# Kernel tuning notes

Measured on AMD Instinct MI355X. Metric: run time of the kernel, lower is better.

The kernel has to match this reference:

```python
import jax, jax.numpy as jnp
import numpy as np

# Action space: 3 discrete action types, 8 options each (MultiDiscrete nvec)
ACTION_NUMS = np.array([8, 8, 8])
A_TOTAL = int(ACTION_NUMS.sum())          # 24
START_IDX = np.cumsum([0, *ACTION_NUMS[:-1]])  # [0, 8, 16]
F, N, D = 4096, 64, 256                   # frames, agents(actions per frame), feat_size
HID = 140                                 # fixed in ForwardNet


def setup_inputs() -> dict:
    key = jax.random.key(0)
    ks = jax.random.split(key, 8)
    s = lambda fan_in: 1.0 / np.sqrt(fan_in)
    return {
        "current_feature": jax.random.normal(ks[0], (F, N, D), jnp.float32),
        "next_feature": jax.random.normal(ks[1], (F, N, D), jnp.float32),
        "actions": jax.random.randint(ks[2], (F, 3, N), 0, 8, dtype=jnp.int32),
        "W1": jax.random.normal(ks[3], (D + A_TOTAL, HID), jnp.float32) * s(D + A_TOTAL),
        "b1": jnp.zeros((HID,), jnp.float32),
        "W2": jax.random.normal(ks[4], (HID, D), jnp.float32) * s(HID),
        "b2": jnp.zeros((D,), jnp.float32),
        "Wi": jax.random.normal(ks[5], (2 * D, A_TOTAL), jnp.float32) * s(2 * D),
        "bi": jnp.zeros((A_TOTAL,), jnp.float32),
    }


def actions2onehot(actions):
    # actions: [F, T, N] int. Vectorized replacement for the triple Python loop:
    # each (frame, agent) row gets a 1 at START_IDX[type] + action, per type.
    start = jnp.asarray(START_IDX, actions.dtype)          # [T]
    idx = actions + start[None, :, None]                    # [F, T, N]
    oh = jax.nn.one_hot(idx, A_TOTAL, dtype=jnp.float32)    # [F, T, N, A]
    return oh.sum(axis=1)                                   # [F, N, A] (column ranges disjoint)


def reference(current_feature, next_feature, actions, W1, b1, W2, b2, Wi, bi):
    action_one_hot = actions2onehot(actions)                       # [F, N, 24]
    # Forward dynamics (attn_target != ICM branch)
    fwd_in = jnp.concatenate([current_feature, action_one_hot], axis=2)  # [F, N, 280]
    h = jax.nn.leaky_relu(fwd_in @ W1 + b1, negative_slope=0.1)
    next_feature_pred = h @ W2 + b2                                # [F, N, 256]
    # Inverse dynamics
    inv_in = jnp.concatenate([current_feature, next_feature], axis=2)   # [F, N, 512]
    action_pred = inv_in @ Wi + bi                                 # [F, N, 24] per-type logits concatenated
    return next_feature_pred, action_pred
```

## Files before the change

kernel.cpp:

```cpp
#include <hip/hip_runtime.h>
#include <hip/hip_bf16.h>
#include <stdint.h>


typedef __attribute__((ext_vector_type(8))) short short8;
typedef __attribute__((ext_vector_type(4))) float float4v;

#define MFMA16 __builtin_amdgcn_mfma_f32_16x16x32_bf16

__device__ __align__(16) uint16_t g_wpack[98816];

__device__ __forceinline__ uint16_t f2bf(float f) {
    __hip_bfloat16 h = __float2bfloat16(f);
    return *reinterpret_cast<uint16_t*>(&h);
}

__device__ __forceinline__ short8 cvt8(float4v x0, float4v x1) {
    union { __hip_bfloat162 b2[4]; short8 s; } u;
    u.b2[0] = __float22bfloat162_rn(make_float2(x0[0], x0[1]));
    u.b2[1] = __float22bfloat162_rn(make_float2(x0[2], x0[3]));
    u.b2[2] = __float22bfloat162_rn(make_float2(x1[0], x1[1]));
    u.b2[3] = __float22bfloat162_rn(make_float2(x1[2], x1[3]));
    return u.s;
}

__global__ __launch_bounds__(256) void pack_weights(
    const float* __restrict__ W1, const float* __restrict__ W2,
    const float* __restrict__ Wi)
{
    int e = blockIdx.x * 256 + threadIdx.x;
    const float* W; int NT, Kr, Nr, ld, le, base;
    if (e < 41472)      { W = W1; NT = 9;  Kr = 280; Nr = 140; ld = 140; le = e;         base = 0; }
    else if (e < 82432) { W = W2; NT = 16; Kr = 140; Nr = 256; ld = 256; le = e - 41472; base = 41472; }
    else if (e < 98816) { W = Wi; NT = 2;  Kr = 512; Nr = 24;  ld = 24;  le = e - 82432; base = 82432; }
    else return;
    int i = le & 7, lane = (le >> 3) & 63, frag = le >> 9;
    int kt = frag / NT, nt = frag - kt * NT;
    int k = kt * 32 + ((lane >> 4) << 3) + i;
    int n = nt * 16 + (lane & 15);
    float v = (k < Kr && n < Nr) ? W[k * ld + n] : 0.0f;
    g_wpack[base + le] = f2bf(v);
}

__global__ __launch_bounds__(256, 2) void icm_main(
    const float* __restrict__ cf, const float* __restrict__ nf,
    const int* __restrict__ act,
    const float* __restrict__ b1, const float* __restrict__ b2,
    const float* __restrict__ bi,
    float* __restrict__ out)
{
    __shared__ char smem[73728];

    const int tid  = threadIdx.x;
    const int wave = tid >> 6;
    const int lane = tid & 63;
    const int lhi  = lane >> 4;
    const int llo  = lane & 15;
    char* hA   = smem + wave * 8192;
    char* hB   = smem + 32768 + wave * 2048;
    char* wstA = smem + 40960;
    char* wstB = smem + 57344;

    const long rowbase = (long)blockIdx.x * 128 + wave * 32;

    short8 wreg[4];

    auto ld_stage1 = [&](int kt) {
        const char* w1b = (const char*)(g_wpack + kt * 9 * 512);
        const char* wib = (const char*)(g_wpack + 82432 + kt * 2 * 512);
        const int nb = (kt == 8) ? 9216 : 11264;
        #pragma unroll
        for (int k = 0; k < 3; ++k) {
            int b = k * 4096 + tid * 16;
            if (b < nb)
                wreg[k] = (b < 9216) ? *(const short8*)(w1b + b)
                                     : *(const short8*)(wib + (b - 9216));
        }
    };
    auto st_stage1 = [&](char* dst, int kt) {
        const int nb = (kt == 8) ? 9216 : 11264;
        #pragma unroll
        for (int k = 0; k < 3; ++k) {
            int b = k * 4096 + tid * 16;
            if (b < nb) *(short8*)(dst + b) = wreg[k];
        }
    };
    auto ld_stage_c = [&](const uint16_t* src) {
        #pragma unroll
        for (int k = 0; k < 4; ++k)
            wreg[k] = *(const short8*)((const char*)src + k * 4096 + tid * 16);
    };
    auto st_stage_c = [&](char* dst) {
        #pragma unroll
        for (int k = 0; k < 4; ++k)
            *(short8*)(dst + k * 4096 + tid * 16) = wreg[k];
    };

    int i0[2], i1[2], i2[2];
    #pragma unroll
    for (int m = 0; m < 2; ++m) {
        long r = rowbase + m * 16 + llo;
        long f = r >> 6; int n = (int)(r & 63);
        i0[m] = act[(f * 3 + 0) * 64 + n];
        i1[m] = act[(f * 3 + 1) * 64 + n] + 8;
        i2[m] = act[(f * 3 + 2) * 64 + n] + 16;
    }

    const float4v fz = {0.f, 0.f, 0.f, 0.f};
    float4v acc1[2][9];
    float4v acc3[2][2];
    #pragma unroll
    for (int m = 0; m < 2; ++m) {
        #pragma unroll
        for (int n = 0; n < 9; ++n) acc1[m][n] = fz;
        acc3[m][0] = fz; acc3[m][1] = fz;
    }

    const float* cfb[2];
    #pragma unroll
    for (int m = 0; m < 2; ++m)
        cfb[m] = cf + (rowbase + m * 16 + llo) * 256 + lhi * 8;

    float4v pa0[2], pa1[2];
    ld_stage1(0);
    #pragma unroll
    for (int m = 0; m < 2; ++m) {
        pa0[m] = *(const float4v*)(cfb[m]);
        pa1[m] = *(const float4v*)(cfb[m] + 4);
    }
    st_stage1(wstA, 0);
    __syncthreads();

    #pragma unroll 1
    for (int kt = 0; kt < 9; ++kt) {
        if (kt < 8) ld_stage1(kt + 1);
        const char* wb = (kt & 1) ? wstB : wstA;

        short8 a[2];
        if (kt < 8) {
            a[0] = cvt8(pa0[0], pa1[0]);
            a[1] = cvt8(pa0[1], pa1[1]);
            if (kt < 7) {
                #pragma unroll
                for (int m = 0; m < 2; ++m) {
                    pa0[m] = *(const float4v*)(cfb[m] + (kt + 1) * 32);
                    pa1[m] = *(const float4v*)(cfb[m] + (kt + 1) * 32 + 4);
                }
            }
        } else {
            #pragma unroll
            for (int m = 0; m < 2; ++m) {
                #pragma unroll
                for (int i = 0; i < 8; ++i) {
                    int kk = lhi * 8 + i;
                    a[m][i] = (kk == i0[m] || kk == i1[m] || kk == i2[m])
                                  ? (short)0x3F80 : (short)0;
                }
            }
        }

        #pragma unroll
        for (int nt = 0; nt < 9; ++nt) {
            short8 bf = *(const short8*)(wb + (nt << 10) + (lane << 4));
            acc1[0][nt] = MFMA16(a[0], bf, acc1[0][nt], 0, 0, 0);
            acc1[1][nt] = MFMA16(a[1], bf, acc1[1][nt], 0, 0, 0);
        }
        if (kt < 8) {
            #pragma unroll
            for (int nt = 0; nt < 2; ++nt) {
                short8 bf = *(const short8*)(wb + ((9 + nt) << 10) + (lane << 4));
                acc3[0][nt] = MFMA16(a[0], bf, acc3[0][nt], 0, 0, 0);
                acc3[1][nt] = MFMA16(a[1], bf, acc3[1][nt], 0, 0, 0);
            }
            st_stage1(((kt + 1) & 1) ? wstB : wstA, kt + 1);
        }
        __syncthreads();
    }

    ld_stage_c(g_wpack + 82432 + (16 << 9));

    #pragma unroll
    for (int m = 0; m < 2; ++m) {
        #pragma unroll
        for (int nt = 0; nt < 9; ++nt) {
            int col = nt * 16 + llo;
            float bb = b1[col < 140 ? col : 139];
            #pragma unroll
            for (int r = 0; r < 4; ++r) {
                float v = acc1[m][nt][r] + bb;
                v = v > 0.f ? v : 0.1f * v;
                int row = m * 16 + lhi * 4 + r;
                if (nt < 8) {
                    int off = row * 256 + ((col * 2) ^ ((row & 7) << 4));
                    *(uint16_t*)(hA + off) = f2bf(v);
                } else {
                    int off = row * 64 + (((col - 128) * 2) ^ ((row & 3) << 4));
                    *(uint16_t*)(hB + off) = f2bf(v);
                }
            }
        }
    }
    #pragma unroll
    for (int z = 0; z < 4; ++z) {
        int zz  = lane * 4 + z;
        int row = zz >> 3, d = zz & 7;
        int off = row * 64 + ((32 + d * 4) ^ ((row & 3) << 4));
        *(int*)(hB + off) = 0;
    }

    st_stage_c(wstB);

    const float* nfb[2];
    #pragma unroll
    for (int m = 0; m < 2; ++m)
        nfb[m] = nf + (rowbase + m * 16 + llo) * 256 + lhi * 8;
    #pragma unroll
    for (int m = 0; m < 2; ++m) {
        pa0[m] = *(const float4v*)(nfb[m]);
        pa1[m] = *(const float4v*)(nfb[m] + 4);
    }
    __syncthreads();

    ld_stage_c(g_wpack + 41472);
    #pragma unroll 1
    for (int kt = 0; kt < 8; ++kt) {
        short8 a[2];
        a[0] = cvt8(pa0[0], pa1[0]);
        a[1] = cvt8(pa0[1], pa1[1]);
        if (kt < 7) {
            #pragma unroll
            for (int m = 0; m < 2; ++m) {
                pa0[m] = *(const float4v*)(nfb[m] + (kt + 1) * 32);
                pa1[m] = *(const float4v*)(nfb[m] + (kt + 1) * 32 + 4);
            }
        }
        #pragma unroll
        for (int nt = 0; nt < 2; ++nt) {
            short8 bf = *(const short8*)(wstB + (((kt << 1) + nt) << 10) + (lane << 4));
            acc3[0][nt] = MFMA16(a[0], bf, acc3[0][nt], 0, 0, 0);
            acc3[1][nt] = MFMA16(a[1], bf, acc3[1][nt], 0, 0, 0);
        }
    }
    float* out2 = out + 67108864L;
    #pragma unroll
    for (int m = 0; m < 2; ++m) {
        #pragma unroll
        for (int nt = 0; nt < 2; ++nt) {
            int col = nt * 16 + llo;
            if (col < 24) {
                float bb = bi[col];
                #pragma unroll
                for (int r = 0; r < 4; ++r) {
                    long row = rowbase + m * 16 + lhi * 4 + r;
                    out2[row * 24 + col] = acc3[m][nt][r] + bb;
                }
            }
        }
    }
    st_stage_c(wstA);
    __syncthreads();

    float4v acc2[2][16];
    #pragma unroll
    for (int m = 0; m < 2; ++m)
        #pragma unroll
        for (int n = 0; n < 16; ++n) acc2[m][n] = fz;

    #pragma unroll 1
    for (int kt = 0; kt < 5; ++kt) {
        if (kt < 4) ld_stage_c(g_wpack + 41472 + ((kt + 1) << 13));
        const char* wb = (kt & 1) ? wstB : wstA;

        short8 a[2];
        #pragma unroll
        for (int m = 0; m < 2; ++m) {
            int row = m * 16 + llo;
            if (kt < 4) {
                int off = row * 256 + ((kt * 64 + lhi * 16) ^ ((row & 7) << 4));
                a[m] = *(const short8*)(hA + off);
            } else {
                int off = row * 64 + ((lhi * 16) ^ ((row & 3) << 4));
                a[m] = *(const short8*)(hB + off);
            }
        }
        #pragma unroll
        for (int nt = 0; nt < 16; ++nt) {
            short8 bf = *(const short8*)(wb + (nt << 10) + (lane << 4));
            acc2[0][nt] = MFMA16(a[0], bf, acc2[0][nt], 0, 0, 0);
            acc2[1][nt] = MFMA16(a[1], bf, acc2[1][nt], 0, 0, 0);
        }
        if (kt < 4) st_stage_c(((kt + 1) & 1) ? wstB : wstA);
        __syncthreads();
    }

    #pragma unroll
    for (int m = 0; m < 2; ++m) {
        #pragma unroll
        for (int n = 0; n < 16; ++n) {
            int col = n * 16 + llo;
            float bb = b2[col];
            #pragma unroll
            for (int r = 0; r < 4; ++r) {
                long row = rowbase + m * 16 + lhi * 4 + r;
                out[row * 256 + col] = acc2[m][n][r] + bb;
            }
        }
    }
}

extern "C" void kernel_launch(void* const* d_in, const int* in_sizes, int n_in,
                              void* d_out, int out_size, void* d_ws, size_t ws_size,
                              hipStream_t stream) {
    const float *cf = nullptr, *nf = nullptr, *W1 = nullptr, *b1 = nullptr;
    const float *W2 = nullptr, *b2 = nullptr, *Wi = nullptr, *bi = nullptr;
    const int *ac = nullptr;
    for (int i = 0; i < n_in; ++i) {
        int s = in_sizes[i];
        const void* p = d_in[i];
        switch (s) {
            case 67108864: if (!cf) cf = (const float*)p; else nf = (const float*)p; break;
            case 786432:   ac = (const int*)p;   break;
            case 39200:    W1 = (const float*)p; break;
            case 140:      b1 = (const float*)p; break;
            case 35840:    W2 = (const float*)p; break;
            case 256:      b2 = (const float*)p; break;
            case 12288:    Wi = (const float*)p; break;
            case 24:       bi = (const float*)p; break;
            default: break;
        }
    }
    float* ob = (float*)d_out;

    pack_weights<<<386, 256, 0, stream>>>(W1, W2, Wi);
    icm_main<<<2048, 256, 0, stream>>>(cf, nf, ac, b1, b2, bi, ob);
}
```

Measured before the change: 205.2 us.

## Stage weights via direct global-to-LDS loads and double-buffer activation prefetch

Replaces the register round-trip for weight staging (global load into VGPRs, then LDS store) with global_load_lds async copies issued per wave. Activation loads now use two alternating register sets, so rows are prefetched two k-steps ahead, and bias values are hoisted into registers. The one-hot k-step is peeled out of the main loop. This aims to free registers and hide global latency better. The risk is ordering and visibility of the LDS copies, which rely on the existing barriers to be complete.

```diff
diff --git a/kernel.cpp b/kernel.cpp
--- a/kernel.cpp
+++ b/kernel.cpp
@@ -9,6 +9,12 @@
 #define MFMA16 __builtin_amdgcn_mfma_f32_16x16x32_bf16
 
 __device__ __align__(16) uint16_t g_wpack[98816];
+
+__device__ __forceinline__ void gl_lds16(const void* g, void* l) {
+    __builtin_amdgcn_global_load_lds(
+        (const __attribute__((address_space(1))) unsigned int*)g,
+        (__attribute__((address_space(3))) unsigned int*)l, 16, 0, 0);
+}
 
 __device__ __forceinline__ uint16_t f2bf(float f) {
     __hip_bfloat16 h = __float2bfloat16(f);
@@ -62,38 +68,27 @@
     char* wstB = smem + 57344;
 
     const long rowbase = (long)blockIdx.x * 128 + wave * 32;
-
-    short8 wreg[4];
-
-    auto ld_stage1 = [&](int kt) {
-        const char* w1b = (const char*)(g_wpack + kt * 9 * 512);
-        const char* wib = (const char*)(g_wpack + 82432 + kt * 2 * 512);
+    const char* gw = (const char*)g_wpack;
+
+    auto stage1 = [&](char* dst, int kt) {
+        const char* w1b = gw + kt * 9216;
+        const char* wib = gw + 164864 + kt * 2048;
         const int nb = (kt == 8) ? 9216 : 11264;
         #pragma unroll
         for (int k = 0; k < 3; ++k) {
-            int b = k * 4096 + tid * 16;
-            if (b < nb)
-                wreg[k] = (b < 9216) ? *(const short8*)(w1b + b)
-                                     : *(const short8*)(wib + (b - 9216));
+            int b = k * 4096 + wave * 1024;
+            if (b < nb) {
+                const char* src = (b < 9216) ? (w1b + b) : (wib + (b - 9216));
+                gl_lds16(src + lane * 16, dst + b);
+            }
         }
     };
-    auto st_stage1 = [&](char* dst, int kt) {
-        const int nb = (kt == 8) ? 9216 : 11264;
-        #pragma unroll
-        for (int k = 0; k < 3; ++k) {
-            int b = k * 4096 + tid * 16;
-            if (b < nb) *(short8*)(dst + b) = wreg[k];
-        }
-    };
-    auto ld_stage_c = [&](const uint16_t* src) {
-        #pragma unroll
-        for (int k = 0; k < 4; ++k)
-            wreg[k] = *(const short8*)((const char*)src + k * 4096 + tid * 16);
-    };
-    auto st_stage_c = [&](char* dst) {
-        #pragma unroll
-        for (int k = 0; k < 4; ++k)
-            *(short8*)(dst + k * 4096 + tid * 16) = wreg[k];
+    auto stage16 = [&](char* dst, const char* src) {
+        #pragma unroll
+        for (int k = 0; k < 4; ++k) {
+            int b = k * 4096 + wave * 1024;
+            gl_lds16(src + b + lane * 16, dst + b);
+        }
     };
 
     int i0[2], i1[2], i2[2];
@@ -105,6 +100,14 @@
         i1[m] = act[(f * 3 + 1) * 64 + n] + 8;
         i2[m] = act[(f * 3 + 2) * 64 + n] + 16;
     }
+    float bb1[9];
+    #pragma unroll
+    for (int nt = 0; nt < 9; ++nt) {
+        int col = nt * 16 + llo;
+        bb1[nt] = b1[col < 140 ? col : 139];
+    }
+    float bi0 = bi[llo];
+    float bi1 = (llo < 8) ? bi[16 + llo] : 0.f;
 
     const float4v fz = {0.f, 0.f, 0.f, 0.f};
     float4v acc1[2][9];
@@ -121,73 +124,85 @@
     for (int m = 0; m < 2; ++m)
         cfb[m] = cf + (rowbase + m * 16 + llo) * 256 + lhi * 8;
 
-    float4v pa0[2], pa1[2];
-    ld_stage1(0);
+    float4v pa0[2], pa1[2], pb0[2], pb1[2];
+    stage1(wstA, 0);
     #pragma unroll
     for (int m = 0; m < 2; ++m) {
         pa0[m] = *(const float4v*)(cfb[m]);
         pa1[m] = *(const float4v*)(cfb[m] + 4);
-    }
-    st_stage1(wstA, 0);
+        pb0[m] = *(const float4v*)(cfb[m] + 32);
+        pb1[m] = *(const float4v*)(cfb[m] + 36);
+    }
     __syncthreads();
 
     #pragma unroll 1
-    for (int kt = 0; kt < 9; ++kt) {
-        if (kt < 8) ld_stage1(kt + 1);
+    for (int kt = 0; kt < 8; ++kt) {
+        stage1((kt & 1) ? wstA : wstB, kt + 1);
         const char* wb = (kt & 1) ? wstB : wstA;
-
         short8 a[2];
-        if (kt < 8) {
-            a[0] = cvt8(pa0[0], pa1[0]);
-            a[1] = cvt8(pa0[1], pa1[1]);
-            if (kt < 7) {
+        if (kt & 1) { a[0] = cvt8(pb0[0], pb1[0]); a[1] = cvt8(pb0[1], pb1[1]); }
+        else        { a[0] = cvt8(pa0[0], pa1[0]); a[1] = cvt8(pa0[1], pa1[1]); }
+        if (kt <= 5) {
+            int o = (kt + 2) * 32;
+            if (kt & 1) {
                 #pragma unroll
                 for (int m = 0; m < 2; ++m) {
-                    pa0[m] = *(const float4v*)(cfb[m] + (kt + 1) * 32);
-                    pa1[m] = *(const float4v*)(cfb[m] + (kt + 1) * 32 + 4);
-                }
-            }
-        } else {
-            #pragma unroll
-            for (int m = 0; m < 2; ++m) {
-                #pragma unroll
-                for (int i = 0; i < 8; ++i) {
-                    int kk = lhi * 8 + i;
-                    a[m][i] = (kk == i0[m] || kk == i1[m] || kk == i2[m])
-                                  ? (short)0x3F80 : (short)0;
-                }
-            }
-        }
-
+                    pb0[m] = *(const float4v*)(cfb[m] + o);
+                    pb1[m] = *(const float4v*)(cfb[m] + o + 4);
+                }
+            } else {
+                #pragma unroll
+                for (int m = 0; m < 2; ++m) {
+                    pa0[m] = *(const float4v*)(cfb[m] + o);
+                    pa1[m] = *(const float4v*)(cfb[m] + o + 4);
+                }
+            }
+        }
         #pragma unroll
         for (int nt = 0; nt < 9; ++nt) {
             short8 bf = *(const short8*)(wb + (nt << 10) + (lane << 4));
             acc1[0][nt] = MFMA16(a[0], bf, acc1[0][nt], 0, 0, 0);
             acc1[1][nt] = MFMA16(a[1], bf, acc1[1][nt], 0, 0, 0);
         }
-        if (kt < 8) {
+        #pragma unroll
+        for (int nt = 0; nt < 2; ++nt) {
+            short8 bf = *(const short8*)(wb + ((9 + nt) << 10) + (lane << 4));
+            acc3[0][nt] = MFMA16(a[0], bf, acc3[0][nt], 0, 0, 0);
+            acc3[1][nt] = MFMA16(a[1], bf, acc3[1][nt], 0, 0, 0);
+        }
+        __syncthreads();
+    }
+    {
+        short8 a[2];
+        #pragma unroll
+        for (int m = 0; m < 2; ++m) {
             #pragma unroll
-            for (int nt = 0; nt < 2; ++nt) {
-                short8 bf = *(const short8*)(wb + ((9 + nt) << 10) + (lane << 4));
-                acc3[0][nt] = MFMA16(a[0], bf, acc3[0][nt], 0, 0, 0);
-                acc3[1][nt] = MFMA16(a[1], bf, acc3[1][nt], 0, 0, 0);
-            }
-            st_stage1(((kt + 1) & 1) ? wstB : wstA, kt + 1);
-        }
-        __syncthreads();
-    }
-
-    ld_stage_c(g_wpack + 82432 + (16 << 9));
+            for (int i = 0; i < 8; ++i) {
+                int kk = lhi * 8 + i;
+                a[m][i] = (kk == i0[m] || kk == i1[m] || kk == i2[m])
+                              ? (short)0x3F80 : (short)0;
+            }
+        }
+        #pragma unroll
+        for (int nt = 0; nt < 9; ++nt) {
+            short8 bf = *(const short8*)(wstA + (nt << 10) + (lane << 4));
+            acc1[0][nt] = MFMA16(a[0], bf, acc1[0][nt], 0, 0, 0);
+            acc1[1][nt] = MFMA16(a[1], bf, acc1[1][nt], 0, 0, 0);
+        }
+    }
+    __syncthreads();
+
+    stage16(wstB, gw + 164864 + 16384);
+    stage16(wstA, gw + 82944);
 
     #pragma unroll
     for (int m = 0; m < 2; ++m) {
         #pragma unroll
         for (int nt = 0; nt < 9; ++nt) {
             int col = nt * 16 + llo;
-            float bb = b1[col < 140 ? col : 139];
             #pragma unroll
             for (int r = 0; r < 4; ++r) {
-                float v = acc1[m][nt][r] + bb;
+                float v = acc1[m][nt][r] + bb1[nt];
                 v = v > 0.f ? v : 0.1f * v;
                 int row = m * 16 + lhi * 4 + r;
                 if (nt < 8) {
@@ -208,8 +223,6 @@
         *(int*)(hB + off) = 0;
     }
 
-    st_stage_c(wstB);
-
     const float* nfb[2];
     #pragma unroll
     for (int m = 0; m < 2; ++m)
@@ -218,20 +231,30 @@
     for (int m = 0; m < 2; ++m) {
         pa0[m] = *(const float4v*)(nfb[m]);
         pa1[m] = *(const float4v*)(nfb[m] + 4);
+        pb0[m] = *(const float4v*)(nfb[m] + 32);
+        pb1[m] = *(const float4v*)(nfb[m] + 36);
     }
     __syncthreads();
 
-    ld_stage_c(g_wpack + 41472);
     #pragma unroll 1
     for (int kt = 0; kt < 8; ++kt) {
         short8 a[2];
-        a[0] = cvt8(pa0[0], pa1[0]);
-        a[1] = cvt8(pa0[1], pa1[1]);
-        if (kt < 7) {
-            #pragma unroll
-            for (int m = 0; m < 2; ++m) {
-                pa0[m] = *(const float4v*)(nfb[m] + (kt + 1) * 32);
-                pa1[m] = *(const float4v*)(nfb[m] + (kt + 1) * 32 + 4);
+        if (kt & 1) { a[0] = cvt8(pb0[0], pb1[0]); a[1] = cvt8(pb0[1], pb1[1]); }
+        else        { a[0] = cvt8(pa0[0], pa1[0]); a[1] = cvt8(pa0[1], pa1[1]); }
+        if (kt <= 5) {
+            int o = (kt + 2) * 32;
+            if (kt & 1) {
+                #pragma unroll
+                for (int m = 0; m < 2; ++m) {
+                    pb0[m] = *(const float4v*)(nfb[m] + o);
+                    pb1[m] = *(const float4v*)(nfb[m] + o + 4);
+                }
+            } else {
+                #pragma unroll
+                for (int m = 0; m < 2; ++m) {
+                    pa0[m] = *(const float4v*)(nfb[m] + o);
+                    pa1[m] = *(const float4v*)(nfb[m] + o + 4);
+                }
             }
         }
         #pragma unroll
@@ -248,7 +271,7 @@
         for (int nt = 0; nt < 2; ++nt) {
             int col = nt * 16 + llo;
             if (col < 24) {
-                float bb = bi[col];
+                float bb = (nt == 0) ? bi0 : bi1;
                 #pragma unroll
                 for (int r = 0; r < 4; ++r) {
                     long row = rowbase + m * 16 + lhi * 4 + r;
@@ -257,7 +280,6 @@
             }
         }
     }
-    st_stage_c(wstA);
     __syncthreads();
 
     float4v acc2[2][16];
@@ -268,9 +290,8 @@
 
     #pragma unroll 1
     for (int kt = 0; kt < 5; ++kt) {
-        if (kt < 4) ld_stage_c(g_wpack + 41472 + ((kt + 1) << 13));
+        if (kt < 4) stage16((kt & 1) ? wstA : wstB, gw + 82944 + (kt + 1) * 16384);
         const char* wb = (kt & 1) ? wstB : wstA;
-
         short8 a[2];
         #pragma unroll
         for (int m = 0; m < 2; ++m) {
@@ -289,8 +310,7 @@
             acc2[0][nt] = MFMA16(a[0], bf, acc2[0][nt], 0, 0, 0);
             acc2[1][nt] = MFMA16(a[1], bf, acc2[1][nt], 0, 0, 0);
         }
-        if (kt < 4) st_stage_c(((kt + 1) & 1) ? wstB : wstA);
-        __syncthreads();
+        if (kt < 4) __syncthreads();
     }
 
     #pragma unroll
```

Measured after the change: 201.0 us. 1.02x faster.
